# Performance work log

Hardware: AMD Instinct MI355X
Metric: run time of the kernel (lower is better)

## Reference

```python
import jax, jax.numpy as jnp
import numpy as np

GROUPS = 8
EPS = 1e-5
PAD = 2  # kernel_size - 1 ('full' padding for stride-1 transposed conv)


def setup_inputs() -> dict:
    key = jax.random.key(0)
    k_x, k_w = jax.random.split(key)
    x = jax.random.normal(k_x, (16, 24, 24, 24, 64), dtype=jnp.float32)
    conv_kernel = jax.random.normal(k_w, (3, 3, 3, 64, 128), dtype=jnp.float32) * 0.05
    gn_scale = jnp.ones((128,), dtype=jnp.float32)
    gn_bias = jnp.zeros((128,), dtype=jnp.float32)
    return {"x": x, "conv_kernel": conv_kernel, "gn_scale": gn_scale, "gn_bias": gn_bias}


def reference(x, conv_kernel, gn_scale, gn_bias):
    # Stride-1 ConvTranspose3d == regular conv with spatially flipped kernel and 'full' padding.
    k_flipped = jnp.flip(conv_kernel, axis=(0, 1, 2))  # DHWIO
    y = jax.lax.conv_general_dilated(
        x, k_flipped,
        window_strides=(1, 1, 1),
        padding=[(PAD, PAD)] * 3,
        dimension_numbers=("NDHWC", "DHWIO", "NDHWC"),
    )  # [B, D+2, H+2, W+2, C_out]
    y = jax.nn.relu(y)
    B, D, H, W, C = y.shape
    yr = y.reshape(B, D, H, W, GROUPS, C // GROUPS)
    mean = jnp.mean(yr, axis=(1, 2, 3, 5), keepdims=True)
    var = jnp.var(yr, axis=(1, 2, 3, 5), keepdims=True)
    yn = ((yr - mean) * jax.lax.rsqrt(var + EPS)).reshape(B, D, H, W, C)
    return yn * gn_scale + gn_bias
```

## Files before the change

kernel.cpp:

```cpp
#include <hip/hip_runtime.h>

#define N_    16
#define DIN   24
#define DOUT  26
#define CIN   64
#define COUT  128
#define NGRP  8
#define EPS   1e-5f

#define STATS_OFF 0
#define KF_OFF    1024

typedef _Float16 half8_t  __attribute__((ext_vector_type(8)));
typedef float    f32x16_t __attribute__((ext_vector_type(16)));

__global__ __launch_bounds__(256) void convert_k_kernel(
    const float* __restrict__ K, _Float16* __restrict__ Kf, float* __restrict__ stats)
{
    int t = blockIdx.x * 256 + threadIdx.x;
    if (blockIdx.x == 0 && threadIdx.x < N_ * NGRP * 2) stats[threadIdx.x] = 0.0f;
    if (t >= 27 * 4 * 4 * 64) return;
    const int lane = t & 63;
    const int nf   = (t >> 6) & 3;
    const int ckg  = (t >> 8) & 3;
    const int tap  = t >> 10;
    const int ci0  = ckg * 16 + (lane >> 5) * 8;
    const int co   = nf * 32 + (lane & 31);
    half8_t h;
    #pragma unroll
    for (int j = 0; j < 8; ++j)
        h[j] = (_Float16)K[(size_t)(tap * CIN + ci0 + j) * COUT + co];
    *(half8_t*)(Kf + (size_t)t * 8) = h;
}

__global__ __launch_bounds__(256, 4) void conv_mfma_kernel(
    const float* __restrict__ x, const _Float16* __restrict__ Kf,
    float* __restrict__ y, float* __restrict__ stats)
{
    __shared__ __align__(16) _Float16 xs[18 * 28 * 40];
    __shared__ float gsum[NGRP], gsq[NGRP];

    const int bid = blockIdx.x;
    const int n   = bid / (DOUT * 7);
    const int rem = bid % (DOUT * 7);
    const int d   = rem / 7;
    const int hb  = (rem % 7) * 4;
    const int tid = threadIdx.x;

    if (tid < NGRP) { gsum[tid] = 0.0f; gsq[tid] = 0.0f; }

    const int lane = tid & 63;
    const int wv   = tid >> 6;
    const int hp   = wv & 1;
    const int nfp  = wv >> 1;
    const int col  = lane & 31;
    const int hi   = lane >> 5;

    int aofs[3];
    #pragma unroll
    for (int aw = 0; aw < 3; ++aw) {
        int sl = col - aw + 2; if (sl > 27) sl = 27;
        aofs[aw] = sl * 40 + hi * 8;
    }

    f32x16_t acc[2][2];
    #pragma unroll
    for (int mt = 0; mt < 2; ++mt)
        #pragma unroll
        for (int fi = 0; fi < 2; ++fi) acc[mt][fi] = (f32x16_t)(0.0f);

    const _Float16* Kfl = Kf + (size_t)lane * 8;

    for (int ph = 0; ph < 2; ++ph) {
        for (int c = tid; c < 2016; c += 256) {
            const int s    = c / 112;
            const int rr   = c % 112;
            const int slot = rr >> 2;
            const int ch   = rr & 3;
            const int dd = d - s / 6;
            const int hh = hb + (s % 6) - 2;
            const int w  = slot - 2;
            half8_t v = {};
            if (dd >= 0 && dd < DIN && hh >= 0 && hh < DIN && w >= 0 && w < DIN) {
                const float* src = x + ((size_t)(((n * DIN + dd) * DIN + hh) * DIN + w)) * CIN
                                     + ph * 32 + ch * 8;
                const float4 a = *(const float4*)(src);
                const float4 b = *(const float4*)(src + 4);
                v[0] = (_Float16)a.x; v[1] = (_Float16)a.y; v[2] = (_Float16)a.z; v[3] = (_Float16)a.w;
                v[4] = (_Float16)b.x; v[5] = (_Float16)b.y; v[6] = (_Float16)b.z; v[7] = (_Float16)b.w;
            }
            *(half8_t*)(xs + s * 1120 + slot * 40 + ch * 8) = v;
        }
        __syncthreads();

        for (int ad = 0; ad < 3; ++ad) {
            for (int ah = 0; ah < 3; ++ah) {
                const int s0  = (ad * 6 + 2 * hp - ah + 2) * 1120;
                const int s1  = s0 + 1120;
                const int tap = (ad * 3 + ah) * 3;
                #pragma unroll
                for (int aw = 0; aw < 3; ++aw) {
                    const _Float16* Bt = Kfl + (size_t)(((tap + aw) * 4 + ph * 2) * 4 + nfp * 2) * 512;
                    #pragma unroll
                    for (int ck = 0; ck < 2; ++ck) {
                        half8_t a0 = *(const half8_t*)(xs + s0 + aofs[aw] + ck * 16);
                        half8_t a1 = *(const half8_t*)(xs + s1 + aofs[aw] + ck * 16);
                        half8_t b0 = *(const half8_t*)(Bt + (size_t)(ck * 4) * 512);
                        half8_t b1 = *(const half8_t*)(Bt + (size_t)(ck * 4 + 1) * 512);
                        acc[0][0] = __builtin_amdgcn_mfma_f32_32x32x16_f16(a0, b0, acc[0][0], 0, 0, 0);
                        acc[0][1] = __builtin_amdgcn_mfma_f32_32x32x16_f16(a0, b1, acc[0][1], 0, 0, 0);
                        acc[1][0] = __builtin_amdgcn_mfma_f32_32x32x16_f16(a1, b0, acc[1][0], 0, 0, 0);
                        acc[1][1] = __builtin_amdgcn_mfma_f32_32x32x16_f16(a1, b1, acc[1][1], 0, 0, 0);
                    }
                }
            }
        }
        if (ph == 0) __syncthreads();
    }

    #pragma unroll
    for (int mt = 0; mt < 2; ++mt) {
        const int hrow = hb + 2 * hp + mt;
        if (hrow >= DOUT) continue;
        const size_t rowbase = (((size_t)(n * DOUT + d)) * DOUT + hrow) * (DOUT * COUT);
        #pragma unroll
        for (int fi = 0; fi < 2; ++fi) {
            const int fr   = nfp * 2 + fi;
            const int cout = fr * 32 + col;
            float ls = 0.f, lsq = 0.f;
            #pragma unroll
            for (int reg = 0; reg < 16; ++reg) {
                const int wout = (reg & 3) + 8 * (reg >> 2) + 4 * hi;
                float v = fmaxf(acc[mt][fi][reg], 0.0f);
                if (wout < DOUT) {
                    y[rowbase + (size_t)wout * COUT + cout] = v;
                    ls += v; lsq += v * v;
                }
            }
            #pragma unroll
            for (int off = 1; off < 16; off <<= 1) {
                ls  += __shfl_xor(ls, off);
                lsq += __shfl_xor(lsq, off);
            }
            ls  += __shfl_xor(ls, 32);
            lsq += __shfl_xor(lsq, 32);
            if (lane == 0 || lane == 16) {
                const int g = fr * 2 + (col >> 4);
                atomicAdd(&gsum[g], ls);
                atomicAdd(&gsq[g], lsq);
            }
        }
    }
    __syncthreads();
    if (tid < NGRP) {
        atomicAdd(&stats[(n * NGRP + tid) * 2 + 0], gsum[tid]);
        atomicAdd(&stats[(n * NGRP + tid) * 2 + 1], gsq[tid]);
    }
}

__global__ __launch_bounds__(256) void gn_apply_kernel(
    float* __restrict__ y, const float* __restrict__ stats,
    const float* __restrict__ scale, const float* __restrict__ bias)
{
    const int total4 = N_ * DOUT * DOUT * DOUT * (COUT / 4);
    int i = blockIdx.x * 256 + threadIdx.x;
    if (i >= total4) return;

    const int t  = i & 31;
    const int co = t * 4;
    const int g  = t >> 2;
    const int n  = i / (DOUT * DOUT * DOUT * (COUT / 4));

    const float s  = stats[(n * NGRP + g) * 2 + 0];
    const float sq = stats[(n * NGRP + g) * 2 + 1];
    const float invN = 1.0f / (float)(DOUT * DOUT * DOUT * (COUT / NGRP));
    const float mean = s * invN;
    const float var  = sq * invN - mean * mean;
    const float rstd = rsqrtf(var + EPS);

    float4 v = ((float4*)y)[i];
    const float4 sc = *(const float4*)(scale + co);
    const float4 bi = *(const float4*)(bias + co);
    v.x = (v.x - mean) * rstd * sc.x + bi.x;
    v.y = (v.y - mean) * rstd * sc.y + bi.y;
    v.z = (v.z - mean) * rstd * sc.z + bi.z;
    v.w = (v.w - mean) * rstd * sc.w + bi.w;
    ((float4*)y)[i] = v;
}

extern "C" void kernel_launch(void* const* d_in, const int* in_sizes, int n_in,
                              void* d_out, int out_size, void* d_ws, size_t ws_size,
                              hipStream_t stream) {
    const float* x     = (const float*)d_in[0];
    const float* K     = (const float*)d_in[1];
    const float* scale = (const float*)d_in[2];
    const float* bias  = (const float*)d_in[3];
    float* y = (float*)d_out;

    float*    stats = (float*)((char*)d_ws + STATS_OFF);
    _Float16* Kf    = (_Float16*)((char*)d_ws + KF_OFF);

    convert_k_kernel<<<108, 256, 0, stream>>>(K, Kf, stats);
    conv_mfma_kernel<<<N_ * DOUT * 7, 256, 0, stream>>>(x, Kf, y, stats);
    const int total4 = N_ * DOUT * DOUT * DOUT * (COUT / 4);
    gn_apply_kernel<<<(total4 + 255) / 256, 256, 0, stream>>>(y, stats, scale, bias);
}
```

Baseline: 356.7 us.

## Pre-convert input to fp16 and stage tiles via direct global-to-LDS loads

Adds a pass that converts x to fp16 in workspace once. The conv kernel then fills its LDS tile with global_load_lds 16-byte transfers, pointing out-of-bounds positions at a zeroed buffer, and uses an XOR-swizzled LDS layout in place of padding to avoid bank conflicts. This is meant to halve the input bytes each block reads, which matters because every block re-reads overlapping halo rows, and to drop the in-register conversion and VGPR staging. The cost is an extra kernel launch plus a full read and write of x. The new path only runs if the workspace is large enough.

```diff
diff --git a/kernel.cpp b/kernel.cpp
--- a/kernel.cpp
+++ b/kernel.cpp
@@ -9,16 +9,29 @@
 #define EPS   1e-5f
 
 #define STATS_OFF 0
-#define KF_OFF    1024
+#define ZERO_OFF  1024
+#define KF_OFF    1280
+#define XH_OFF    458752
+#define XH_BYTES  ((size_t)N_ * DIN * DIN * DIN * CIN * 2)
+#define XH_END    ((size_t)XH_OFF + XH_BYTES)
 
 typedef _Float16 half8_t  __attribute__((ext_vector_type(8)));
 typedef float    f32x16_t __attribute__((ext_vector_type(16)));
 
+typedef __attribute__((address_space(3))) void       lds_void;
+typedef __attribute__((address_space(1))) const void glb_void;
+
+__device__ __forceinline__ void gload_lds16(const void* g, void* l) {
+    __builtin_amdgcn_global_load_lds((glb_void*)g, (lds_void*)l, 16, 0, 0);
+}
+
 __global__ __launch_bounds__(256) void convert_k_kernel(
-    const float* __restrict__ K, _Float16* __restrict__ Kf, float* __restrict__ stats)
+    const float* __restrict__ K, _Float16* __restrict__ Kf,
+    float* __restrict__ stats, float* __restrict__ zbuf)
 {
     int t = blockIdx.x * 256 + threadIdx.x;
     if (blockIdx.x == 0 && threadIdx.x < N_ * NGRP * 2) stats[threadIdx.x] = 0.0f;
+    if (blockIdx.x == 1 && threadIdx.x < 16) zbuf[threadIdx.x] = 0.0f;
     if (t >= 27 * 4 * 4 * 64) return;
     const int lane = t & 63;
     const int nf   = (t >> 6) & 3;
@@ -31,6 +44,149 @@
     for (int j = 0; j < 8; ++j)
         h[j] = (_Float16)K[(size_t)(tap * CIN + ci0 + j) * COUT + co];
     *(half8_t*)(Kf + (size_t)t * 8) = h;
+}
+
+__global__ __launch_bounds__(256) void convert_x_kernel(
+    const float* __restrict__ x, _Float16* __restrict__ xh)
+{
+    const int TOT = N_ * DIN * DIN * DIN * CIN / 8;
+    int i = blockIdx.x * 256 + threadIdx.x;
+    if (i >= TOT) return;
+    const float4 a = ((const float4*)x)[(size_t)i * 2];
+    const float4 b = ((const float4*)x)[(size_t)i * 2 + 1];
+    half8_t v;
+    v[0] = (_Float16)a.x; v[1] = (_Float16)a.y; v[2] = (_Float16)a.z; v[3] = (_Float16)a.w;
+    v[4] = (_Float16)b.x; v[5] = (_Float16)b.y; v[6] = (_Float16)b.z; v[7] = (_Float16)b.w;
+    *(half8_t*)(xh + (size_t)i * 8) = v;
+}
+
+__global__ __launch_bounds__(256, 4) void conv_mfma_f16x_kernel(
+    const _Float16* __restrict__ xh, const _Float16* __restrict__ Kf,
+    float* __restrict__ y, float* __restrict__ stats, const float* __restrict__ zbuf)
+{
+    __shared__ __align__(16) _Float16 xs[18 * 32 * 32];
+    __shared__ float gsum[NGRP], gsq[NGRP];
+
+    const int bid = blockIdx.x;
+    const int n   = bid / (DOUT * 7);
+    const int rem = bid % (DOUT * 7);
+    const int d   = rem / 7;
+    const int hb  = (rem % 7) * 4;
+    const int tid = threadIdx.x;
+
+    if (tid < NGRP) { gsum[tid] = 0.0f; gsq[tid] = 0.0f; }
+
+    const int lane = tid & 63;
+    const int wv   = tid >> 6;
+    const int hp   = wv & 1;
+    const int nfp  = wv >> 1;
+    const int col  = lane & 31;
+    const int hi   = lane >> 5;
+
+    int ofs[3][2];
+    #pragma unroll
+    for (int aw = 0; aw < 3; ++aw) {
+        int sl = col - aw + 2; if (sl > 31) sl = 31;
+        #pragma unroll
+        for (int ck = 0; ck < 2; ++ck) {
+            const int ch = hi + 2 * ck;
+            ofs[aw][ck] = sl * 64 + ((ch ^ ((sl >> 1) & 3)) * 16);
+        }
+    }
+
+    f32x16_t acc[2][2];
+    #pragma unroll
+    for (int mt = 0; mt < 2; ++mt)
+        #pragma unroll
+        for (int fi = 0; fi < 2; ++fi) acc[mt][fi] = (f32x16_t)(0.0f);
+
+    const char* xsb = (const char*)xs + hp * 4096;
+
+    for (int ph = 0; ph < 2; ++ph) {
+        #pragma unroll
+        for (int k = 0; k < 9; ++k) {
+            const int c    = tid + k * 256;
+            const int s    = c >> 7;
+            const int r    = c & 127;
+            const int slot = r >> 2;
+            const int wch  = r & 3;
+            const int ch   = wch ^ ((slot >> 1) & 3);
+            const int dd = d - s / 6;
+            const int hh = hb + (s % 6) - 2;
+            const int w  = slot - 2;
+            const void* src;
+            if ((unsigned)dd < DIN && (unsigned)hh < DIN && (unsigned)w < DIN)
+                src = xh + ((((size_t)n * DIN + dd) * DIN + hh) * DIN + w) * CIN
+                         + ph * 32 + ch * 8;
+            else
+                src = zbuf;
+            gload_lds16(src, (char*)xs + (size_t)c * 16);
+        }
+        __syncthreads();
+
+        const _Float16* Kfp = Kf + (size_t)lane * 8 + (size_t)(ph * 8 + nfp * 2) * 512;
+        for (int ad = 0; ad < 3; ++ad) {
+            for (int ah = 0; ah < 3; ++ah) {
+                const int s0b = (ad * 6 - ah + 2) * 2048;
+                const int tap = (ad * 3 + ah) * 3;
+                #pragma unroll
+                for (int aw = 0; aw < 3; ++aw) {
+                    const _Float16* Bt = Kfp + (size_t)((tap + aw) * 16) * 512;
+                    #pragma unroll
+                    for (int ck = 0; ck < 2; ++ck) {
+                        half8_t a0 = *(const half8_t*)(xsb + s0b + ofs[aw][ck]);
+                        half8_t a1 = *(const half8_t*)(xsb + s0b + 2048 + ofs[aw][ck]);
+                        half8_t b0 = *(const half8_t*)(Bt + (size_t)(ck * 4) * 512);
+                        half8_t b1 = *(const half8_t*)(Bt + (size_t)(ck * 4 + 1) * 512);
+                        acc[0][0] = __builtin_amdgcn_mfma_f32_32x32x16_f16(a0, b0, acc[0][0], 0, 0, 0);
+                        acc[0][1] = __builtin_amdgcn_mfma_f32_32x32x16_f16(a0, b1, acc[0][1], 0, 0, 0);
+                        acc[1][0] = __builtin_amdgcn_mfma_f32_32x32x16_f16(a1, b0, acc[1][0], 0, 0, 0);
+                        acc[1][1] = __builtin_amdgcn_mfma_f32_32x32x16_f16(a1, b1, acc[1][1], 0, 0, 0);
+                    }
+                }
+            }
+        }
+        if (ph == 0) __syncthreads();
+    }
+
+    #pragma unroll
+    for (int mt = 0; mt < 2; ++mt) {
+        const int hrow = hb + 2 * hp + mt;
+        if (hrow >= DOUT) continue;
+        const size_t rowbase = (((size_t)(n * DOUT + d)) * DOUT + hrow) * (DOUT * COUT);
+        #pragma unroll
+        for (int fi = 0; fi < 2; ++fi) {
+            const int fr   = nfp * 2 + fi;
+            const int cout = fr * 32 + col;
+            float ls = 0.f, lsq = 0.f;
+            #pragma unroll
+            for (int reg = 0; reg < 16; ++reg) {
+                const int wout = (reg & 3) + 8 * (reg >> 2) + 4 * hi;
+                float v = fmaxf(acc[mt][fi][reg], 0.0f);
+                if (wout < DOUT) {
+                    y[rowbase + (size_t)wout * COUT + cout] = v;
+                    ls += v; lsq += v * v;
+                }
+            }
+            #pragma unroll
+            for (int off = 1; off < 16; off <<= 1) {
+                ls  += __shfl_xor(ls, off);
+                lsq += __shfl_xor(lsq, off);
+            }
+            ls  += __shfl_xor(ls, 32);
+            lsq += __shfl_xor(lsq, 32);
+            if (lane == 0 || lane == 16) {
+                const int g = fr * 2 + (col >> 4);
+                atomicAdd(&gsum[g], ls);
+                atomicAdd(&gsq[g], lsq);
+            }
+        }
+    }
+    __syncthreads();
+    if (tid < NGRP) {
+        atomicAdd(&stats[(n * NGRP + tid) * 2 + 0], gsum[tid]);
+        atomicAdd(&stats[(n * NGRP + tid) * 2 + 1], gsq[tid]);
+    }
 }
 
 __global__ __launch_bounds__(256, 4) void conv_mfma_kernel(
@@ -198,10 +354,20 @@
     float* y = (float*)d_out;
 
     float*    stats = (float*)((char*)d_ws + STATS_OFF);
+    float*    zbuf  = (float*)((char*)d_ws + ZERO_OFF);
     _Float16* Kf    = (_Float16*)((char*)d_ws + KF_OFF);
-
-    convert_k_kernel<<<108, 256, 0, stream>>>(K, Kf, stats);
-    conv_mfma_kernel<<<N_ * DOUT * 7, 256, 0, stream>>>(x, Kf, y, stats);
+    _Float16* xh    = (_Float16*)((char*)d_ws + XH_OFF);
+
+    convert_k_kernel<<<108, 256, 0, stream>>>(K, Kf, stats, zbuf);
+
+    if (ws_size >= XH_END) {
+        const int xtot = N_ * DIN * DIN * DIN * CIN / 8;
+        convert_x_kernel<<<(xtot + 255) / 256, 256, 0, stream>>>(x, xh);
+        conv_mfma_f16x_kernel<<<N_ * DOUT * 7, 256, 0, stream>>>(xh, Kf, y, stats, zbuf);
+    } else {
+        conv_mfma_kernel<<<N_ * DOUT * 7, 256, 0, stream>>>(x, Kf, y, stats);
+    }
+
     const int total4 = N_ * DOUT * DOUT * DOUT * (COUT / 4);
     gn_apply_kernel<<<(total4 + 255) / 256, 256, 0, stream>>>(y, stats, scale, bias);
 }
```

New measurement: 389.8 us. 9.3% more time.

## Give each wave one output-channel fragment across four rows, and swizzle block order

Applied to the files above, without the earlier changes.

Each wave now owns one 32-wide output-channel fragment and all four output H rows. One weight fragment load therefore feeds four MFMAs, where before a 2x2 layout needed two A and two B loads per four MFMAs. This cuts global/L2 weight traffic per MFMA and adds LDS activation reads. Block indices are also remapped in strides of eight, likely to spread neighbouring blocks across XCDs or cache domains. The workspace offset for the converted kernel moves slightly.

```diff
diff --git a/kernel.cpp b/kernel.cpp
--- a/kernel.cpp
+++ b/kernel.cpp
@@ -9,7 +9,7 @@
 #define EPS   1e-5f
 
 #define STATS_OFF 0
-#define KF_OFF    1024
+#define KF_OFF    1280
 
 typedef _Float16 half8_t  __attribute__((ext_vector_type(8)));
 typedef float    f32x16_t __attribute__((ext_vector_type(16)));
@@ -40,7 +40,9 @@
     __shared__ __align__(16) _Float16 xs[18 * 28 * 40];
     __shared__ float gsum[NGRP], gsq[NGRP];
 
-    const int bid = blockIdx.x;
+    int bid = blockIdx.x;
+    bid = (bid & 7) * ((N_ * DOUT * 7) >> 3) + (bid >> 3);
+
     const int n   = bid / (DOUT * 7);
     const int rem = bid % (DOUT * 7);
     const int d   = rem / 7;
@@ -51,8 +53,6 @@
 
     const int lane = tid & 63;
     const int wv   = tid >> 6;
-    const int hp   = wv & 1;
-    const int nfp  = wv >> 1;
     const int col  = lane & 31;
     const int hi   = lane >> 5;
 
@@ -63,13 +63,11 @@
         aofs[aw] = sl * 40 + hi * 8;
     }
 
-    f32x16_t acc[2][2];
+    f32x16_t acc[4];
     #pragma unroll
-    for (int mt = 0; mt < 2; ++mt)
-        #pragma unroll
-        for (int fi = 0; fi < 2; ++fi) acc[mt][fi] = (f32x16_t)(0.0f);
+    for (int q = 0; q < 4; ++q) acc[q] = (f32x16_t)(0.0f);
 
-    const _Float16* Kfl = Kf + (size_t)lane * 8;
+    const _Float16* Kfl = Kf + (size_t)lane * 8 + (size_t)wv * 512;
 
     for (int ph = 0; ph < 2; ++ph) {
         for (int c = tid; c < 2016; c += 256) {
@@ -94,23 +92,21 @@
         __syncthreads();
 
         for (int ad = 0; ad < 3; ++ad) {
+            #pragma unroll
             for (int ah = 0; ah < 3; ++ah) {
-                const int s0  = (ad * 6 + 2 * hp - ah + 2) * 1120;
-                const int s1  = s0 + 1120;
+                const int sb  = (ad * 6 - ah + 2) * 1120;
                 const int tap = (ad * 3 + ah) * 3;
                 #pragma unroll
                 for (int aw = 0; aw < 3; ++aw) {
-                    const _Float16* Bt = Kfl + (size_t)(((tap + aw) * 4 + ph * 2) * 4 + nfp * 2) * 512;
                     #pragma unroll
                     for (int ck = 0; ck < 2; ++ck) {
-                        half8_t a0 = *(const half8_t*)(xs + s0 + aofs[aw] + ck * 16);
-                        half8_t a1 = *(const half8_t*)(xs + s1 + aofs[aw] + ck * 16);
-                        half8_t b0 = *(const half8_t*)(Bt + (size_t)(ck * 4) * 512);
-                        half8_t b1 = *(const half8_t*)(Bt + (size_t)(ck * 4 + 1) * 512);
-                        acc[0][0] = __builtin_amdgcn_mfma_f32_32x32x16_f16(a0, b0, acc[0][0], 0, 0, 0);
-                        acc[0][1] = __builtin_amdgcn_mfma_f32_32x32x16_f16(a0, b1, acc[0][1], 0, 0, 0);
-                        acc[1][0] = __builtin_amdgcn_mfma_f32_32x32x16_f16(a1, b0, acc[1][0], 0, 0, 0);
-                        acc[1][1] = __builtin_amdgcn_mfma_f32_32x32x16_f16(a1, b1, acc[1][1], 0, 0, 0);
+                        half8_t b = *(const half8_t*)(
+                            Kfl + (size_t)(((tap + aw) * 4 + ph * 2 + ck) * 4) * 512);
+                        #pragma unroll
+                        for (int q = 0; q < 4; ++q) {
+                            half8_t a = *(const half8_t*)(xs + sb + q * 1120 + aofs[aw] + ck * 16);
+                            acc[q] = __builtin_amdgcn_mfma_f32_32x32x16_f16(a, b, acc[q], 0, 0, 0);
+                        }
                     }
                 }
             }
@@ -119,36 +115,32 @@
     }
 
     #pragma unroll
-    for (int mt = 0; mt < 2; ++mt) {
-        const int hrow = hb + 2 * hp + mt;
+    for (int q = 0; q < 4; ++q) {
+        const int hrow = hb + q;
         if (hrow >= DOUT) continue;
         const size_t rowbase = (((size_t)(n * DOUT + d)) * DOUT + hrow) * (DOUT * COUT);
+        const int cout = wv * 32 + col;
+        float ls = 0.f, lsq = 0.f;
         #pragma unroll
-        for (int fi = 0; fi < 2; ++fi) {
-            const int fr   = nfp * 2 + fi;
-            const int cout = fr * 32 + col;
-            float ls = 0.f, lsq = 0.f;
-            #pragma unroll
-            for (int reg = 0; reg < 16; ++reg) {
-                const int wout = (reg & 3) + 8 * (reg >> 2) + 4 * hi;
-                float v = fmaxf(acc[mt][fi][reg], 0.0f);
-                if (wout < DOUT) {
-                    y[rowbase + (size_t)wout * COUT + cout] = v;
-                    ls += v; lsq += v * v;
-                }
+        for (int reg = 0; reg < 16; ++reg) {
+            const int wout = (reg & 3) + 8 * (reg >> 2) + 4 * hi;
+            float v = fmaxf(acc[q][reg], 0.0f);
+            if (wout < DOUT) {
+                y[rowbase + (size_t)wout * COUT + cout] = v;
+                ls += v; lsq += v * v;
             }
-            #pragma unroll
-            for (int off = 1; off < 16; off <<= 1) {
-                ls  += __shfl_xor(ls, off);
-                lsq += __shfl_xor(lsq, off);
-            }
-            ls  += __shfl_xor(ls, 32);
-            lsq += __shfl_xor(lsq, 32);
-            if (lane == 0 || lane == 16) {
-                const int g = fr * 2 + (col >> 4);
-                atomicAdd(&gsum[g], ls);
-                atomicAdd(&gsq[g], lsq);
-            }
+        }
+        #pragma unroll
+        for (int off = 1; off < 16; off <<= 1) {
+            ls  += __shfl_xor(ls, off);
+            lsq += __shfl_xor(lsq, off);
+        }
+        ls  += __shfl_xor(ls, 32);
+        lsq += __shfl_xor(lsq, 32);
+        if (lane == 0 || lane == 16) {
+            const int g = wv * 2 + (col >> 4);
+            atomicAdd(&gsum[g], ls);
+            atomicAdd(&gsq[g], lsq);
         }
     }
     __syncthreads();
```

Result: slower. 538.4 us (+50.9%).
